# Kernel optimization log

Measured on AMD Instinct MI355X. Metric: run time of the kernel, lower is better.

Reference implementation:

```python
import jax, jax.numpy as jnp
import numpy as np

V, E, H, K, B, T = 50000, 300, 256, 25, 64, 256


def setup_inputs() -> dict:
    key = jax.random.key(0)
    ks = jax.random.split(key, 20)
    g = lambda k, shape, s=0.05: (jax.random.normal(k, shape, dtype=jnp.float32) * s)
    return {
        "sentence": jax.random.randint(ks[0], (B, T), 0, V),
        "labels": jax.random.randint(ks[1], (B, T), 0, K),
        "mask": jnp.ones((B, T), dtype=bool),
        "emb_table": g(ks[2], (V, E), 0.1),
        "w_ih_f": g(ks[3], (4 * H, E)),
        "w_hh_f": g(ks[4], (4 * H, H)),
        "b_ih_f": g(ks[5], (4 * H,)),
        "b_hh_f": g(ks[6], (4 * H,)),
        "w_ih_b": g(ks[7], (4 * H, E)),
        "w_hh_b": g(ks[8], (4 * H, H)),
        "b_ih_b": g(ks[9], (4 * H,)),
        "b_hh_b": g(ks[10], (4 * H,)),
        "W_out": g(ks[11], (K, 2 * H)),
        "b_out": g(ks[12], (K,)),
        "start_trans": g(ks[13], (K,), 0.1),
        "end_trans": g(ks[14], (K,), 0.1),
        "trans": g(ks[15], (K, K), 0.1),
    }


def _lstm_dir(x, w_ih, w_hh, b_ih, b_hh, reverse):
    # x: [T, B, E] -> hs: [T, B, H]; torch gate order i,f,g,o
    xg = jnp.einsum('tbe,ge->tbg', x, w_ih) + b_ih + b_hh  # [T,B,4H]
    h0 = jnp.zeros((x.shape[1], w_hh.shape[1]), x.dtype)

    def step(carry, g_t):
        h, c = carry
        gates = g_t + h @ w_hh.T
        i, f, gg, o = jnp.split(gates, 4, axis=-1)
        c = jax.nn.sigmoid(f) * c + jax.nn.sigmoid(i) * jnp.tanh(gg)
        h = jax.nn.sigmoid(o) * jnp.tanh(c)
        return (h, c), h

    _, hs = jax.lax.scan(step, (h0, h0), xg, reverse=reverse)
    return hs


def _crf_nll(emissions, labels, mask, start_trans, end_trans, trans):
    # emissions: [B,T,K]; returns sum over batch of -(log-likelihood)
    maskf = mask.astype(emissions.dtype)
    # --- numerator: score of the gold path ---
    em_sc = jnp.take_along_axis(emissions, labels[..., None], axis=-1)[..., 0]  # [B,T]
    tr_sc = trans[labels[:, :-1], labels[:, 1:]]  # [B,T-1]
    seq_ends = jnp.sum(mask.astype(jnp.int32), axis=1) - 1  # [B]
    last_tags = jnp.take_along_axis(labels, seq_ends[:, None], axis=1)[:, 0]
    num = (start_trans[labels[:, 0]] + em_sc[:, 0]
           + jnp.sum((em_sc[:, 1:] + tr_sc) * maskf[:, 1:], axis=1)
           + end_trans[last_tags])  # [B]
    # --- denominator: forward algorithm (sequential logsumexp scan) ---
    alpha0 = start_trans + emissions[:, 0]  # [B,K]
    em_rest = emissions[:, 1:].transpose(1, 0, 2)  # [T-1,B,K]
    m_rest = maskf[:, 1:].T  # [T-1,B]

    def step(alpha, xs):
        e_t, m_t = xs
        nxt = jax.nn.logsumexp(alpha[:, :, None] + trans[None] + e_t[:, None, :], axis=1)
        alpha = jnp.where(m_t[:, None] > 0, nxt, alpha)
        return alpha, None

    alpha, _ = jax.lax.scan(step, alpha0, (em_rest, m_rest))
    logZ = jax.nn.logsumexp(alpha + end_trans, axis=-1)  # [B]
    return jnp.sum(logZ - num)


def reference(sentence, labels, mask, emb_table,
              w_ih_f, w_hh_f, b_ih_f, b_hh_f,
              w_ih_b, w_hh_b, b_ih_b, b_hh_b,
              W_out, b_out, start_trans, end_trans, trans):
    x = emb_table[sentence].transpose(1, 0, 2)  # [T,B,E]
    hf = _lstm_dir(x, w_ih_f, w_hh_f, b_ih_f, b_hh_f, reverse=False)
    hb = _lstm_dir(x, w_ih_b, w_hh_b, b_ih_b, b_hh_b, reverse=True)
    h = jnp.concatenate([hf, hb], axis=-1)  # [T,B,2H]  (dropout = identity, eval)
    emissions = (h @ W_out.T + b_out).transpose(1, 0, 2)  # [B,T,K]
    return _crf_nll(emissions, labels, mask, start_trans, end_trans, trans)
```

## Files before the change

kernel.cpp:

```cpp
#include <hip/hip_runtime.h>
#include <math.h>

#define B_ 64
#define T_ 256
#define E_ 300
#define EP 160
#define H_ 256
#define K_ 25
#define G4 1024
#define M_ (B_*T_)

#define QL 18
#define QS 14

typedef _Float16 h2v __attribute__((ext_vector_type(2)));
typedef _Float16 f16x8 __attribute__((ext_vector_type(8)));
typedef float f32x4 __attribute__((ext_vector_type(4)));

__device__ __forceinline__ float sigm(float x) {
    return __builtin_amdgcn_rcpf(1.0f + __expf(-x));
}
__device__ __forceinline__ float tanhfast(float x) {
    return 1.0f - 2.0f * __builtin_amdgcn_rcpf(1.0f + __expf(2.0f * x));
}
__device__ __forceinline__ h2v asH2(unsigned u) { return __builtin_bit_cast(h2v, u); }
__device__ __forceinline__ unsigned pack_h2(float a, float b) {
    union { _Float16 h[2]; unsigned u; } cv;
    cv.h[0] = (_Float16)a; cv.h[1] = (_Float16)b; return cv.u;
}
__device__ __forceinline__ unsigned short f16u(float a) {
    union { _Float16 h; unsigned short u; } cv; cv.h = (_Float16)a; return cv.u;
}

__global__ __launch_bounds__(256) void prep_kernel(
    const float* __restrict__ w_ih_f, const float* __restrict__ b_ih_f,
    const float* __restrict__ b_hh_f, const float* __restrict__ w_ih_b,
    const float* __restrict__ b_ih_b, const float* __restrict__ b_hh_b,
    const float* __restrict__ W_out,
    unsigned* __restrict__ wPt, unsigned short* __restrict__ wE,
    float* __restrict__ biasC)
{
    int idx = blockIdx.x * 256 + threadIdx.x;
    if (idx < 2*G4*EP) {
        int ng = idx / EP, kp = idx - ng*EP;
        int d = ng >> 10, n = ng & 1023;
        int u = n >> 2, g = n & 3;
        const float* w = d ? w_ih_b : w_ih_f;
        float a = 0.f, bb = 0.f;
        if (kp < 150) { a = w[(g*H_+u)*E_ + 2*kp]; bb = w[(g*H_+u)*E_ + 2*kp + 1]; }
        wPt[idx] = pack_h2(a, bb);
    }
    if (idx < K_*2*H_) wE[idx] = f16u(W_out[idx]);
    if (idx < 2*G4) {
        int d = idx >> 10; int n = idx & 1023;
        int u = n >> 2, g = n & 3;
        biasC[idx] = d ? (b_ih_b[g*H_+u] + b_hh_b[g*H_+u])
                       : (b_ih_f[g*H_+u] + b_hh_f[g*H_+u]);
    }
}

__global__ __launch_bounds__(256) void scale_kernel(
    const float* __restrict__ w_hh_f, const float* __restrict__ w_hh_b,
    float* __restrict__ swF)
{
    int row = blockIdx.x*4 + (threadIdx.x >> 6);
    int lane = threadIdx.x & 63;
    int d = row >> 10, rr = row & 1023;
    const float* w = (d ? w_hh_b : w_hh_f) + (size_t)rr*H_;
    float m = 0.f;
    #pragma unroll
    for (int q = 0; q < 4; q++) m = fmaxf(m, fabsf(w[lane + q*64]));
    #pragma unroll
    for (int off = 32; off; off >>= 1) m = fmaxf(m, __shfl_down(m, off));
    if (lane == 0) {
        int g = rr >> 8, j = rr & 255;
        swF[(d*H_ + j)*4 + g] = fmaxf(m, 1e-20f) / 127.f;
    }
}

__global__ __launch_bounds__(256) void quant_kernel(
    const float* __restrict__ w_hh_f, const float* __restrict__ w_hh_b,
    const float* __restrict__ swF, uint4* __restrict__ wqL, uint4* __restrict__ wqS)
{
    int idx = blockIdx.x*256 + threadIdx.x;
    if (idx >= 2*64*256) return;
    int d = idx >> 14, q = (idx >> 8) & 63, j = idx & 255;
    const float* w = d ? w_hh_b : w_hh_f;
    unsigned words[4];
    #pragma unroll
    for (int g = 0; g < 4; g++) {
        float s = swF[(d*H_ + j)*4 + g];
        unsigned wd = 0;
        #pragma unroll
        for (int kk = 0; kk < 4; kk++) {
            float v = w[(size_t)(g*H_ + j)*H_ + 4*q + kk] / s;
            int q8 = (int)__builtin_rintf(v);
            q8 = q8 > 127 ? 127 : (q8 < -127 ? -127 : q8);
            wd |= ((unsigned)(q8 & 0xFF)) << (8*kk);
        }
        words[g] = wd;
    }
    uint4 W = make_uint4(words[0], words[1], words[2], words[3]);
    int kh = q >> 5, qq = q & 31;
    if (qq < QL) wqL[((size_t)d*2*QL + kh*QL + qq)*256 + j] = W;
    else         wqS[((size_t)d*2*QS + kh*QS + (qq-QL))*256 + j] = W;
}

__global__ __launch_bounds__(256) void gather_kernel(const int* __restrict__ sent,
    const float* __restrict__ emb, unsigned* __restrict__ xP)
{
    int idx = blockIdx.x * 256 + threadIdx.x;
    if (idx >= EP*M_) return;
    int tb = idx / EP;
    int kp = idx - tb*EP;
    unsigned v = 0;
    if (kp < 150) {
        const float* er = emb + (size_t)sent[tb]*E_;
        v = pack_h2(er[2*kp], er[2*kp+1]);
    }
    xP[idx] = v;
}

__global__ __launch_bounds__(256) void gemm_xg_kernel(const unsigned* __restrict__ xP,
    const unsigned* __restrict__ wPt, const float* __restrict__ biasC,
    unsigned* __restrict__ xgu)
{
    __shared__ __align__(16) char smem[33792];
    unsigned (*As)[20] = (unsigned(*)[20])smem;
    unsigned (*Bs)[20] = (unsigned(*)[20])(smem + 10240);
    unsigned (*Cs)[66] = (unsigned(*)[66])smem;

    int bx = blockIdx.x & 15;
    int by = blockIdx.x >> 4;
    int row0 = by*128, col0 = bx*128;
    int d = col0 >> 10, g0 = col0 & 1023;
    int tid = threadIdx.x;
    int lane = tid & 63, wid = tid >> 6;
    int wm = wid >> 1, wn = wid & 1;
    int lg = lane >> 4, lr = lane & 15;

    int r0 = tid >> 2, q0 = tid & 3;
    int r1 = r0 + 64;
    const unsigned* gA0 = xP  + (size_t)(row0 + r0)*EP + q0*4;
    const unsigned* gA1 = xP  + (size_t)(row0 + r1)*EP + q0*4;
    const unsigned* gB0 = wPt + (size_t)(d*1024 + g0 + r0)*EP + q0*4;
    const unsigned* gB1 = wPt + (size_t)(d*1024 + g0 + r1)*EP + q0*4;

    f32x4 acc[4][4];
    #pragma unroll
    for (int i = 0; i < 4; i++)
        #pragma unroll
        for (int jj = 0; jj < 4; jj++) acc[i][jj] = (f32x4){0.f,0.f,0.f,0.f};

    uint4 ra0 = *(const uint4*)gA0, ra1 = *(const uint4*)gA1;
    uint4 rb0 = *(const uint4*)gB0, rb1 = *(const uint4*)gB1;

    #pragma unroll 1
    for (int it = 0; it < 10; ++it) {
        __syncthreads();
        *(uint4*)&As[r0][q0*4] = ra0;  *(uint4*)&As[r1][q0*4] = ra1;
        *(uint4*)&Bs[r0][q0*4] = rb0;  *(uint4*)&Bs[r1][q0*4] = rb1;
        __syncthreads();
        if (it < 9) {
            int off = (it+1)*16;
            ra0 = *(const uint4*)(gA0 + off); ra1 = *(const uint4*)(gA1 + off);
            rb0 = *(const uint4*)(gB0 + off); rb1 = *(const uint4*)(gB1 + off);
        }
        union U { uint4 u; f16x8 v; };
        U af[4], bf[4];
        #pragma unroll
        for (int f = 0; f < 4; f++) {
            af[f].u = *(const uint4*)&As[wm*64 + f*16 + lr][lg*4];
            bf[f].u = *(const uint4*)&Bs[wn*64 + f*16 + lr][lg*4];
        }
        #pragma unroll
        for (int fm = 0; fm < 4; fm++)
            #pragma unroll
            for (int fn = 0; fn < 4; fn++)
                acc[fm][fn] = __builtin_amdgcn_mfma_f32_16x16x32_f16(
                    bf[fn].v, af[fm].v, acc[fm][fn], 0, 0, 0);
    }
    __syncthreads();
    #pragma unroll
    for (int fn = 0; fn < 4; fn++) {
        int n4 = wn*64 + fn*16 + lg*4;
        float b0 = biasC[d*G4 + g0 + n4],     b1 = biasC[d*G4 + g0 + n4 + 1];
        float b2 = biasC[d*G4 + g0 + n4 + 2], b3 = biasC[d*G4 + g0 + n4 + 3];
        #pragma unroll
        for (int fm = 0; fm < 4; fm++) {
            int row = wm*64 + fm*16 + lr;
            Cs[row][(n4>>1)]     = pack_h2(acc[fm][fn][0] + b0, acc[fm][fn][1] + b1);
            Cs[row][(n4>>1) + 1] = pack_h2(acc[fm][fn][2] + b2, acc[fm][fn][3] + b3);
        }
    }
    __syncthreads();
    for (int i = tid; i < 128*64; i += 256) {
        int r = i >> 6, cc = i & 63;
        xgu[((size_t)d*M_ + row0 + r)*512 + (g0 >> 1) + cc] = Cs[r][cc];
    }
}

__global__ __launch_bounds__(512, 2) void lstm_kernel(
    const uint4* __restrict__ wqL, const uint4* __restrict__ wqS,
    const float4* __restrict__ swF4, const unsigned* __restrict__ xgu,
    unsigned short* __restrict__ hs16)
{
    int blk = blockIdx.x;
    int d = blk >> 6, b = blk & 63;
    int tid = threadIdx.x;
    int kh = tid >> 8, j = tid & 255;

    __shared__ uint4 wlds[2*QL][256];
    __shared__ int4 part[256];
    __shared__ __align__(16) unsigned hq[64];

    for (int i = tid; i < 2*QS*256; i += 512)
        wlds[i >> 8][i & 255] = wqS[(size_t)d*2*QS*256 + i];
    __syncthreads();
    uint4 rv[QS];
    #pragma unroll
    for (int s = 0; s < QS; s++) rv[s] = wlds[kh*QS + s][j];
    __syncthreads();
    for (int i = tid; i < 2*QL*256; i += 512)
        wlds[i >> 8][i & 255] = wqL[(size_t)d*2*QL*256 + i];
    if (tid < 64) hq[tid] = 0u;

    const unsigned* xgp = xgu + ((size_t)d*M_ + (size_t)b*T_)*512;
    unsigned short* hsp = hs16 + ((size_t)(d*B_ + b)*T_)*H_;
    int t0 = d ? T_-1 : 0;
    int dt = d ? -1 : 1;
    float4 sc = make_float4(0.f,0.f,0.f,0.f);
    uint2 xw = make_uint2(0u, 0u);
    if (!kh) {
        float4 s0 = ((const float4*)swF4)[d*H_ + j];
        sc = make_float4(s0.x*(1.f/127.f), s0.y*(1.f/127.f),
                         s0.z*(1.f/127.f), s0.w*(1.f/127.f));
        xw = *(const uint2*)&xgp[t0*512 + 2*j];
    }
    float c = 0.f;
    __syncthreads();

    int t = t0;
    #pragma unroll 1
    for (int tt = 0; tt < T_; tt++) {
        int a0 = 0, a1 = 0, a2 = 0, a3 = 0;
        const uint4* hb = ((const uint4*)hq) + kh*8;
        #pragma unroll
        for (int qg = 0; qg < 8; qg++) {
            uint4 hw4 = hb[qg];
            #pragma unroll
            for (int e = 0; e < 4; e++) {
                int ql = qg*4 + e;
                unsigned hw = (e==0)?hw4.x:(e==1)?hw4.y:(e==2)?hw4.z:hw4.w;
                uint4 w4 = (ql < QL) ? wlds[kh*QL + ql][j] : rv[ql - QL];
                a0 = __builtin_amdgcn_sdot4((int)w4.x, (int)hw, a0, false);
                a1 = __builtin_amdgcn_sdot4((int)w4.y, (int)hw, a1, false);
                a2 = __builtin_amdgcn_sdot4((int)w4.z, (int)hw, a2, false);
                a3 = __builtin_amdgcn_sdot4((int)w4.w, (int)hw, a3, false);
            }
        }
        if (kh) part[j] = make_int4(a0, a1, a2, a3);
        __syncthreads();
        if (!kh) {
            int4 p1 = part[j];
            h2v x01 = asH2(xw.x), x23 = asH2(xw.y);
            float gi = (float)(a0 + p1.x)*sc.x + (float)x01[0];
            float gf = (float)(a1 + p1.y)*sc.y + (float)x01[1];
            float gg = (float)(a2 + p1.z)*sc.z + (float)x23[0];
            float go = (float)(a3 + p1.w)*sc.w + (float)x23[1];
            c = sigm(gf)*c + sigm(gi)*tanhfast(gg);
            float h = sigm(go)*tanhfast(c);
            hsp[(size_t)t*H_ + j] = f16u(h);
            int q8 = (int)__builtin_rintf(h * 127.f);
            ((char*)hq)[j] = (char)q8;
            if (tt < T_-1) xw = *(const uint2*)&xgp[(t+dt)*512 + 2*j];
        }
        t += dt;
        __syncthreads();
    }
}

__global__ __launch_bounds__(256) void emis_kernel(const unsigned short* __restrict__ hs16,
    const unsigned short* __restrict__ wE, const float* __restrict__ b_out,
    float* __restrict__ em)
{
    int idx = blockIdx.x*256 + threadIdx.x;
    if (idx >= M_*K_) return;
    int tb = idx / K_, k = idx % K_;
    const uint4* hf = (const uint4*)(hs16 + (size_t)tb*H_);
    const uint4* hb = (const uint4*)(hs16 + (size_t)B_*T_*H_ + (size_t)tb*H_);
    const uint4* w0 = (const uint4*)(wE + (size_t)k*2*H_);
    float s = b_out[k];
    #pragma unroll 8
    for (int q = 0; q < 32; q++) {
        uint4 h = hf[q], w = w0[q];
        s = __builtin_amdgcn_fdot2(asH2(h.x), asH2(w.x), s, false);
        s = __builtin_amdgcn_fdot2(asH2(h.y), asH2(w.y), s, false);
        s = __builtin_amdgcn_fdot2(asH2(h.z), asH2(w.z), s, false);
        s = __builtin_amdgcn_fdot2(asH2(h.w), asH2(w.w), s, false);
    }
    #pragma unroll 8
    for (int q = 0; q < 32; q++) {
        uint4 h = hb[q], w = w0[32+q];
        s = __builtin_amdgcn_fdot2(asH2(h.x), asH2(w.x), s, false);
        s = __builtin_amdgcn_fdot2(asH2(h.y), asH2(w.y), s, false);
        s = __builtin_amdgcn_fdot2(asH2(h.z), asH2(w.z), s, false);
        s = __builtin_amdgcn_fdot2(asH2(h.w), asH2(w.w), s, false);
    }
    em[idx] = s;
}

__global__ void zero_kernel(float* out) { out[0] = 0.f; }

__global__ __launch_bounds__(64) void crf_kernel(const float* __restrict__ em,
    const int* __restrict__ labels, const float* __restrict__ start_t,
    const float* __restrict__ end_t, const float* __restrict__ trans,
    float* __restrict__ out)
{
    int b = blockIdx.x, lane = threadIdx.x;
    const int* lab = labels + b*T_;
    const float* emr = em + (size_t)b*T_*K_;

    float part = 0.f;
    for (int t = lane; t < T_; t += 64) {
        int lt = lab[t];
        part += emr[t*K_ + lt];
        part += (t == 0) ? start_t[lt] : trans[lab[t-1]*K_ + lt];
    }
    if (lane == 0) part += end_t[lab[T_-1]];
    #pragma unroll
    for (int off = 32; off; off >>= 1) part += __shfl_down(part, off);

    bool act = lane < K_;
    float trc[K_];
    #pragma unroll
    for (int i = 0; i < K_; i++) trc[i] = act ? trans[i*K_ + lane] : 0.f;
    float alpha = act ? (start_t[lane] + emr[lane]) : -1e30f;
    float ej = act ? emr[K_ + lane] : 0.f;
    #pragma unroll 1
    for (int t = 1; t < T_; t++) {
        float ej_next = (t+1 < T_ && act) ? emr[(t+1)*K_ + lane] : 0.f;
        float vals[K_];
        #pragma unroll
        for (int i = 0; i < K_; i++) {
            float ai = __shfl(alpha, i);
            vals[i] = ai + trc[i];
        }
        float mx[16];
        #pragma unroll
        for (int i = 0; i < 16; i++) mx[i] = vals[i];
        #pragma unroll
        for (int i = 16; i < K_; i++) mx[i-16] = fmaxf(mx[i-16], vals[i]);
        #pragma unroll
        for (int s2 = 8; s2 >= 1; s2 >>= 1)
            #pragma unroll
            for (int i = 0; i < s2; i++) mx[i] = fmaxf(mx[i], mx[i+s2]);
        float m = mx[0];
        float ev[16];
        #pragma unroll
        for (int i = 0; i < 16; i++) ev[i] = __expf(vals[i] - m);
        #pragma unroll
        for (int i = 16; i < K_; i++) ev[i-16] += __expf(vals[i] - m);
        #pragma unroll
        for (int s2 = 8; s2 >= 1; s2 >>= 1)
            #pragma unroll
            for (int i = 0; i < s2; i++) ev[i] += ev[i+s2];
        float na = __logf(ev[0]) + m + ej;
        alpha = act ? na : -1e30f;
        ej = ej_next;
    }
    float v = act ? (alpha + end_t[lane]) : -1e30f;
    float m = v;
    #pragma unroll
    for (int off = 32; off; off >>= 1) m = fmaxf(m, __shfl_down(m, off));
    m = __shfl(m, 0);
    float s = act ? __expf(v - m) : 0.f;
    #pragma unroll
    for (int off = 32; off; off >>= 1) s += __shfl_down(s, off);
    if (lane == 0) {
        float logZ = __logf(s) + m;
        atomicAdd(out, logZ - part);
    }
}

extern "C" void kernel_launch(void* const* d_in, const int* in_sizes, int n_in,
                              void* d_out, int out_size, void* d_ws, size_t ws_size,
                              hipStream_t stream)
{
    const int*   sentence = (const int*)  d_in[0];
    const int*   labels   = (const int*)  d_in[1];
    const float* emb      = (const float*)d_in[3];
    const float* w_ih_f   = (const float*)d_in[4];
    const float* w_hh_f   = (const float*)d_in[5];
    const float* b_ih_f   = (const float*)d_in[6];
    const float* b_hh_f   = (const float*)d_in[7];
    const float* w_ih_b   = (const float*)d_in[8];
    const float* w_hh_b   = (const float*)d_in[9];
    const float* b_ih_b   = (const float*)d_in[10];
    const float* b_hh_b   = (const float*)d_in[11];
    const float* W_out    = (const float*)d_in[12];
    const float* b_out    = (const float*)d_in[13];
    const float* start_t  = (const float*)d_in[14];
    const float* end_t    = (const float*)d_in[15];
    const float* trans    = (const float*)d_in[16];

    char* ws = (char*)d_ws;
    unsigned*       xP   = (unsigned*)      (ws);
    unsigned*       xgu  = (unsigned*)      (ws + 10485760);
    unsigned*       wPt  = (unsigned*)      (ws + 77594624);
    float*          swF  = (float*)         (ws + 78905344);
    uint4*          wqL  = (uint4*)         (ws + 78913536);
    uint4*          wqS  = (uint4*)         (ws + 79208448);
    float*          biasC= (float*)         (ws + 79437824);
    unsigned short* wE   = (unsigned short*)(ws + 79446016);
    unsigned short* hs16 = (unsigned short*)(ws + 79471616);
    float*          em   = (float*)         (ws + 96248832);

    prep_kernel<<<1280, 256, 0, stream>>>(w_ih_f, b_ih_f, b_hh_f,
                                          w_ih_b, b_ih_b, b_hh_b, W_out,
                                          wPt, wE, biasC);
    scale_kernel<<<512, 256, 0, stream>>>(w_hh_f, w_hh_b, swF);
    quant_kernel<<<128, 256, 0, stream>>>(w_hh_f, w_hh_b, swF, wqL, wqS);
    gather_kernel<<<(EP*M_)/256, 256, 0, stream>>>(sentence, emb, xP);
    gemm_xg_kernel<<<128*16, 256, 0, stream>>>(xP, wPt, biasC, xgu);
    lstm_kernel<<<128, 512, 0, stream>>>(wqL, wqS, (const float4*)swF, xgu, hs16);
    emis_kernel<<<(M_*K_ + 255)/256, 256, 0, stream>>>(hs16, wE, b_out, em);
    zero_kernel<<<1, 1, 0, stream>>>((float*)d_out);
    crf_kernel<<<B_, 64, 0, stream>>>(em, labels, start_t, end_t, trans, (float*)d_out);
}
```

Before: 501.2 us.

## Split recurrent weights across LDS, registers, and per-step global streaming

The LSTM recurrent int8 weights are split three ways: 9 rows per half stay in LDS, 14 in registers, and 9 are re-read from global/L2 each timestep. A 32 KB LDS padding array is added, apparently to force one block per CU so each block gets the whole CU's bandwidth. The h vector is preloaded into registers before the dot products. The change trades LDS capacity and occupancy for per-step global loads, which add latency on the serial recurrence.

```diff
diff --git a/kernel.cpp b/kernel.cpp
--- a/kernel.cpp
+++ b/kernel.cpp
@@ -10,8 +10,9 @@
 #define G4 1024
 #define M_ (B_*T_)
 
-#define QL 18
-#define QS 14
+#define PLDS 9
+#define PREG 14
+#define PSTR 9
 
 typedef _Float16 h2v __attribute__((ext_vector_type(2)));
 typedef _Float16 f16x8 __attribute__((ext_vector_type(8)));
@@ -80,7 +81,8 @@
 
 __global__ __launch_bounds__(256) void quant_kernel(
     const float* __restrict__ w_hh_f, const float* __restrict__ w_hh_b,
-    const float* __restrict__ swF, uint4* __restrict__ wqL, uint4* __restrict__ wqS)
+    const float* __restrict__ swF, uint4* __restrict__ wqL,
+    uint4* __restrict__ wqS, uint4* __restrict__ wqV)
 {
     int idx = blockIdx.x*256 + threadIdx.x;
     if (idx >= 2*64*256) return;
@@ -102,8 +104,12 @@
     }
     uint4 W = make_uint4(words[0], words[1], words[2], words[3]);
     int kh = q >> 5, qq = q & 31;
-    if (qq < QL) wqL[((size_t)d*2*QL + kh*QL + qq)*256 + j] = W;
-    else         wqS[((size_t)d*2*QS + kh*QS + (qq-QL))*256 + j] = W;
+    if (qq < PLDS)
+        wqL[((size_t)d*2*PLDS + kh*PLDS + qq)*256 + j] = W;
+    else if (qq < PLDS+PREG)
+        wqS[((size_t)d*2*PREG + kh*PREG + (qq-PLDS))*256 + j] = W;
+    else
+        wqV[((size_t)d*2*PSTR + kh*PSTR + (qq-PLDS-PREG))*256 + j] = W;
 }
 
 __global__ __launch_bounds__(256) void gather_kernel(const int* __restrict__ sent,
@@ -202,29 +208,40 @@
 
 __global__ __launch_bounds__(512, 2) void lstm_kernel(
     const uint4* __restrict__ wqL, const uint4* __restrict__ wqS,
-    const float4* __restrict__ swF4, const unsigned* __restrict__ xgu,
-    unsigned short* __restrict__ hs16)
+    const uint4* __restrict__ wqV, const float4* __restrict__ swF4,
+    const unsigned* __restrict__ xgu, unsigned short* __restrict__ hs16)
 {
     int blk = blockIdx.x;
     int d = blk >> 6, b = blk & 63;
     int tid = threadIdx.x;
     int kh = tid >> 8, j = tid & 255;
 
-    __shared__ uint4 wlds[2*QL][256];
+    __shared__ uint4 wlds[2*PLDS][256];
     __shared__ int4 part[256];
     __shared__ __align__(16) unsigned hq[64];
-
-    for (int i = tid; i < 2*QS*256; i += 512)
-        wlds[i >> 8][i & 255] = wqS[(size_t)d*2*QS*256 + i];
-    __syncthreads();
-    uint4 rv[QS];
-    #pragma unroll
-    for (int s = 0; s < QS; s++) rv[s] = wlds[kh*QS + s][j];
-    __syncthreads();
-    for (int i = tid; i < 2*QL*256; i += 512)
-        wlds[i >> 8][i & 255] = wqL[(size_t)d*2*QL*256 + i];
+    __shared__ float ldspad[8192];
+    if (tid == 0) ldspad[0] = 0.f;
+
+    uint4 rv[PREG];
+    #pragma unroll 1
+    for (int pass = 0; pass < 2; pass++) {
+        int base = pass * 2*PLDS;
+        int nrows = (2*PREG - base) < 2*PLDS ? (2*PREG - base) : 2*PLDS;
+        for (int i = tid; i < nrows*256; i += 512)
+            wlds[i >> 8][i & 255] = wqS[(size_t)d*2*PREG*256 + ((size_t)base << 8) + i];
+        __syncthreads();
+        #pragma unroll
+        for (int s = 0; s < PREG; s++) {
+            int r = kh*PREG + s;
+            if (r >= base && r < base + nrows) rv[s] = wlds[r - base][j];
+        }
+        __syncthreads();
+    }
+    for (int i = tid; i < 2*PLDS*256; i += 512)
+        wlds[i >> 8][i & 255] = wqL[(size_t)d*2*PLDS*256 + i];
     if (tid < 64) hq[tid] = 0u;
 
+    const uint4* wVp = wqV + ((size_t)(d*2 + kh)*PSTR)*256 + j;
     const unsigned* xgp = xgu + ((size_t)d*M_ + (size_t)b*T_)*512;
     unsigned short* hsp = hs16 + ((size_t)(d*B_ + b)*T_)*H_;
     int t0 = d ? T_-1 : 0;
@@ -243,21 +260,48 @@
     int t = t0;
     #pragma unroll 1
     for (int tt = 0; tt < T_; tt++) {
+        asm volatile("" : "+v"(wVp));
+        uint4 sv[PSTR];
+        #pragma unroll
+        for (int v = 0; v < PSTR; v++) sv[v] = wVp[(size_t)v*256];
+
+        uint4 hb[8];
+        const uint4* hbase = ((const uint4*)hq) + kh*8;
+        #pragma unroll
+        for (int qg = 0; qg < 8; qg++) hb[qg] = hbase[qg];
+
         int a0 = 0, a1 = 0, a2 = 0, a3 = 0;
-        const uint4* hb = ((const uint4*)hq) + kh*8;
-        #pragma unroll
-        for (int qg = 0; qg < 8; qg++) {
-            uint4 hw4 = hb[qg];
-            #pragma unroll
-            for (int e = 0; e < 4; e++) {
-                int ql = qg*4 + e;
-                unsigned hw = (e==0)?hw4.x:(e==1)?hw4.y:(e==2)?hw4.z:hw4.w;
-                uint4 w4 = (ql < QL) ? wlds[kh*QL + ql][j] : rv[ql - QL];
-                a0 = __builtin_amdgcn_sdot4((int)w4.x, (int)hw, a0, false);
-                a1 = __builtin_amdgcn_sdot4((int)w4.y, (int)hw, a1, false);
-                a2 = __builtin_amdgcn_sdot4((int)w4.z, (int)hw, a2, false);
-                a3 = __builtin_amdgcn_sdot4((int)w4.w, (int)hw, a3, false);
-            }
+        #pragma unroll
+        for (int ql = 0; ql < PLDS; ql++) {
+            uint4 vv = hb[ql>>2];
+            unsigned hw = ((ql&3)==0)?vv.x:((ql&3)==1)?vv.y:((ql&3)==2)?vv.z:vv.w;
+            uint4 w4 = wlds[kh*PLDS + ql][j];
+            a0 = __builtin_amdgcn_sdot4((int)w4.x, (int)hw, a0, false);
+            a1 = __builtin_amdgcn_sdot4((int)w4.y, (int)hw, a1, false);
+            a2 = __builtin_amdgcn_sdot4((int)w4.z, (int)hw, a2, false);
+            a3 = __builtin_amdgcn_sdot4((int)w4.w, (int)hw, a3, false);
+        }
+        #pragma unroll
+        for (int s = 0; s < PREG; s++) {
+            int ql = PLDS + s;
+            uint4 vv = hb[ql>>2];
+            unsigned hw = ((ql&3)==0)?vv.x:((ql&3)==1)?vv.y:((ql&3)==2)?vv.z:vv.w;
+            uint4 w4 = rv[s];
+            a0 = __builtin_amdgcn_sdot4((int)w4.x, (int)hw, a0, false);
+            a1 = __builtin_amdgcn_sdot4((int)w4.y, (int)hw, a1, false);
+            a2 = __builtin_amdgcn_sdot4((int)w4.z, (int)hw, a2, false);
+            a3 = __builtin_amdgcn_sdot4((int)w4.w, (int)hw, a3, false);
+        }
+        #pragma unroll
+        for (int v = 0; v < PSTR; v++) {
+            int ql = PLDS + PREG + v;
+            uint4 vv = hb[ql>>2];
+            unsigned hw = ((ql&3)==0)?vv.x:((ql&3)==1)?vv.y:((ql&3)==2)?vv.z:vv.w;
+            uint4 w4 = sv[v];
+            a0 = __builtin_amdgcn_sdot4((int)w4.x, (int)hw, a0, false);
+            a1 = __builtin_amdgcn_sdot4((int)w4.y, (int)hw, a1, false);
+            a2 = __builtin_amdgcn_sdot4((int)w4.z, (int)hw, a2, false);
+            a3 = __builtin_amdgcn_sdot4((int)w4.w, (int)hw, a3, false);
         }
         if (kh) part[j] = make_int4(a0, a1, a2, a3);
         __syncthreads();
@@ -410,7 +454,8 @@
     unsigned*       wPt  = (unsigned*)      (ws + 77594624);
     float*          swF  = (float*)         (ws + 78905344);
     uint4*          wqL  = (uint4*)         (ws + 78913536);
-    uint4*          wqS  = (uint4*)         (ws + 79208448);
+    uint4*          wqS  = (uint4*)         (ws + 79060992);
+    uint4*          wqV  = (uint4*)         (ws + 79290368);
     float*          biasC= (float*)         (ws + 79437824);
     unsigned short* wE   = (unsigned short*)(ws + 79446016);
     unsigned short* hs16 = (unsigned short*)(ws + 79471616);
@@ -420,10 +465,10 @@
                                           w_ih_b, b_ih_b, b_hh_b, W_out,
                                           wPt, wE, biasC);
     scale_kernel<<<512, 256, 0, stream>>>(w_hh_f, w_hh_b, swF);
-    quant_kernel<<<128, 256, 0, stream>>>(w_hh_f, w_hh_b, swF, wqL, wqS);
+    quant_kernel<<<128, 256, 0, stream>>>(w_hh_f, w_hh_b, swF, wqL, wqS, wqV);
     gather_kernel<<<(EP*M_)/256, 256, 0, stream>>>(sentence, emb, xP);
     gemm_xg_kernel<<<128*16, 256, 0, stream>>>(xP, wPt, biasC, xgu);
-    lstm_kernel<<<128, 512, 0, stream>>>(wqL, wqS, (const float4*)swF, xgu, hs16);
+    lstm_kernel<<<128, 512, 0, stream>>>(wqL, wqS, wqV, (const float4*)swF, xgu, hs16);
     emis_kernel<<<(M_*K_ + 255)/256, 256, 0, stream>>>(hs16, wE, b_out, em);
     zero_kernel<<<1, 1, 0, stream>>>((float*)d_out);
     crf_kernel<<<B_, 64, 0, stream>>>(em, labels, start_t, end_t, trans, (float*)d_out);
```

Measured after the change: 578.7 us. +15.5%, slower.
